# Kernel tuning notes

Measured on AMD Instinct MI355X. Metric: run time of the kernel, lower is better.

## Reference

```python
import jax, jax.numpy as jnp
import numpy as np

HEADS = 8
DIM_HEAD = 64
SCALE = DIM_HEAD ** (-0.5)


def setup_inputs() -> dict:
    key = jax.random.key(0)
    k1, k2, k3 = jax.random.split(key, 3)
    b, l, c = 8, 4096, 512
    x = jax.random.normal(k1, (b, l, c), dtype=jnp.float32)
    w_qkv = jax.random.normal(k2, (3 * c, c), dtype=jnp.float32) * (c ** -0.5)
    w_out = jax.random.normal(k3, (c, c), dtype=jnp.float32) * (c ** -0.5)
    b_out = jnp.zeros((c,), dtype=jnp.float32)
    return {"x": x, "w_qkv": w_qkv, "w_out": w_out, "b_out": b_out}


def reference(x, w_qkv, w_out, b_out):
    b, l, c = x.shape
    h = HEADS
    lh = l // h
    # to_qkv: Linear(dim, 3*dim, bias=False)
    qkv = x @ w_qkv.T                                   # (b, l, 3c)
    qkv = qkv.reshape(b, lh, h, 3, c).transpose(3, 0, 2, 1, 4)  # (3, b, h, l/h, c)
    q, k, v = qkv[0], qkv[1], qkv[2]                    # each (b, h, l/h, c)
    # transpose(-2,-1): attention is over the CHANNEL axis
    q = jnp.swapaxes(q, -2, -1)                         # (b, h, c, l/h)
    k = jnp.swapaxes(k, -2, -1)                         # (b, h, c, l/h)
    v = jnp.swapaxes(v, -2, -1)                         # (b, h, c, l/h)
    attn = jnp.einsum('bhcl,bhdl->bhcd', q, k) * SCALE  # (b, h, c, c)
    attn = jax.nn.softmax(attn, axis=-1)
    y = jnp.einsum('bhcd,bhdl->bhcl', attn, v)          # (b, h, c, l/h)
    y = y.transpose(0, 3, 1, 2).reshape(b, l, c)        # (b, l/h, h, c) -> (b, l, c)
    # to_out: Linear(dim, dim) + Dropout (identity at eval)
    out = y @ w_out.T + b_out
    return out
```

## Files before the change

kernel.cpp:

```cpp
#include <hip/hip_runtime.h>
#include <stdint.h>
#include <stddef.h>

typedef _Float16 f16;
typedef _Float16 f16x8 __attribute__((ext_vector_type(8)));
typedef _Float16 f16x4 __attribute__((ext_vector_type(4)));
typedef float f32x4 __attribute__((ext_vector_type(4)));

__device__ __forceinline__ void gload16(const void* g, void* l) {
    auto gp = (const __attribute__((address_space(1))) uint32_t*)(uintptr_t)g;
    auto lp = (__attribute__((address_space(3))) uint32_t*)(uintptr_t)l;
    __builtin_amdgcn_global_load_lds(gp, lp, 16, 0, 0);
}

__device__ __forceinline__ f16x4 cvt4(f32x4 v) {
    return f16x4{ (f16)v[0], (f16)v[1], (f16)v[2], (f16)v[3] };
}

__global__ __launch_bounds__(256) void prep_k(const float* __restrict__ x,
                                              const float* __restrict__ wqkv,
                                              const float* __restrict__ wout,
                                              f16* __restrict__ xb,
                                              f16* __restrict__ wqb,
                                              f16* __restrict__ wob) {
    int tid = blockIdx.x * blockDim.x + threadIdx.x;
    int stride = gridDim.x * blockDim.x;
    for (int i = tid; i < 4194304; i += stride) {
        float4 v = ((const float4*)x)[i];
        *(f16x4*)(xb + (size_t)i * 4) = f16x4{ (f16)v.x, (f16)v.y, (f16)v.z, (f16)v.w };
    }
    for (int i = tid; i < 196608; i += stride) {
        float4 v = ((const float4*)wqkv)[i];
        *(f16x4*)(wqb + (size_t)i * 4) = f16x4{ (f16)v.x, (f16)v.y, (f16)v.z, (f16)v.w };
    }
    for (int i = tid; i < 65536; i += stride) {
        float4 v = ((const float4*)wout)[i];
        *(f16x4*)(wob + (size_t)i * 4) = f16x4{ (f16)v.x, (f16)v.y, (f16)v.z, (f16)v.w };
    }
}


#define STAGE(NB) do {                                                          \
    gload16(Ab + kb + sE,          &ldsA[NB][( 0 + wid*8)*64]);                 \
    gload16(Ab + kb + sO + 32768,  &ldsA[NB][(32 + wid*8)*64]);                 \
    gload16(Ab + kb + sE + 65536,  &ldsA[NB][(64 + wid*8)*64]);                 \
    gload16(Ab + kb + sO + 98304,  &ldsA[NB][(96 + wid*8)*64]);                 \
    gload16(Bb + kb + sE,          &ldsB[NB][( 0 + wid*8)*64]);                 \
    gload16(Bb + kb + sO + 32768,  &ldsB[NB][(32 + wid*8)*64]);                 \
    gload16(Bb + kb + sE + 65536,  &ldsB[NB][(64 + wid*8)*64]);                 \
    gload16(Bb + kb + sO + 98304,  &ldsB[NB][(96 + wid*8)*64]);                 \
    kb += 128;                                                                  \
} while (0)

#define RD(SET, BUF) do {                                                       \
    _Pragma("unroll") for (int mi = 0; mi < 4; ++mi)                            \
    _Pragma("unroll") for (int kk = 0; kk < 2; ++kk)                            \
        aF##SET[mi][kk] = *(const f16x8*)(&ldsA[BUF][0] + aoff[mi][kk]);        \
    _Pragma("unroll") for (int ni = 0; ni < 4; ++ni)                            \
    _Pragma("unroll") for (int kk = 0; kk < 2; ++kk)                            \
        bF##SET[ni][kk] = *(const f16x8*)(&ldsB[BUF][0] + boff[ni][kk]);        \
} while (0)

#define MM(SET, KK, ML, MH_) do {                                               \
    __builtin_amdgcn_s_setprio(1);                                              \
    _Pragma("unroll") for (int mi = ML; mi < MH_; ++mi)                         \
    _Pragma("unroll") for (int ni = 0; ni < 4; ++ni) {                          \
        if constexpr (SWP)                                                      \
            acc[mi][ni] = __builtin_amdgcn_mfma_f32_16x16x32_f16(               \
                bF##SET[ni][KK], aF##SET[mi][KK], acc[mi][ni], 0, 0, 0);        \
        else                                                                    \
            acc[mi][ni] = __builtin_amdgcn_mfma_f32_16x16x32_f16(               \
                aF##SET[mi][KK], bF##SET[ni][KK], acc[mi][ni], 0, 0, 0);        \
    }                                                                           \
    __builtin_amdgcn_s_setprio(0);                                              \
} while (0)

#define MM3(SET)   do { MM(SET, 0, 0, 2); MM(SET, 0, 2, 4); MM(SET, 1, 0, 2); } while (0)
#define MMLAST(SET) MM(SET, 1, 2, 4)
#define W0  asm volatile("s_waitcnt vmcnt(0)" ::: "memory")
#define BAR __builtin_amdgcn_s_barrier()

#define TILE(CUR, NXT, NB, STG, FINAL) do {                                     \
    if (STG) STAGE(NB);                                                         \
    MM3(CUR);                                                                   \
    if (!FINAL) { W0; BAR; RD(NXT, NB); }                                       \
    MMLAST(CUR);                                                                \
} while (0)

template <int MODE, bool SWP, bool QK>
__global__ __launch_bounds__(256, 2) void g10_k(const f16* __restrict__ A0,
                                                const f16* __restrict__ B0,
                                                void* __restrict__ C0,
                                                void* __restrict__ C1,
                                                const float* __restrict__ bias) {
    __shared__ f16 ldsA[2][8192];
    __shared__ f16 ldsB[2][8192];

    const int tid = threadIdx.x;
    const int lane = tid & 63;
    const int wid = tid >> 6;
    const int wr = wid >> 1;
    const int wc = wid & 1;

    const int bid = blockIdx.x;
    int tm, tn, bh = 0;
    if constexpr (MODE == 0 && QK) {
        int swz = (bid & 7) * 256 + (bid >> 3);
        tm = (swz >> 3) * 128; tn = (swz & 7) * 128;
    } else if constexpr (MODE == 0) {
        int swz = (bid & 7) * 128 + (bid >> 3);
        tm = (swz >> 2) * 128; tn = (swz & 3) * 128;
    } else if constexpr (MODE == 1 || MODE == 2) {
        int swz = (bid & 7) * 128 + (bid >> 3);
        bh = swz >> 4; tm = ((swz >> 2) & 3) * 128; tn = (swz & 3) * 128;
    } else {
        int swz = (bid & 7) * 128 + (bid >> 3);
        tm = (swz >> 2) * 128; tn = (swz & 3) * 128;
    }

    const size_t bhoff = (MODE == 1 || MODE == 2) ? (size_t)bh * 262144 : 0;
    const char* Ab = (const char*)(A0 + bhoff + (size_t)tm * 512);
    const char* Bb = (const char*)(B0 + bhoff + (size_t)tn * 512);

    const int u = tid >> 3;
    const int colE = ((tid & 7) ^ ((u & 7) ^ (u >> 3))) * 16;
    const int sE = u * 1024 + colE;
    const int sO = sE ^ 64;
    int kb = 0;

    int aoff[4][2], boff[4][2];
#pragma unroll
    for (int mi = 0; mi < 4; ++mi) {
        int r;
        if constexpr (QK) {
            r = (lane & 15) * 8 + wr * 4 + mi;
        } else {
            r = wr * 64 + mi * 16 + (lane & 15);
        }
#pragma unroll
        for (int kk = 0; kk < 2; ++kk) {
            int c8 = (lane >> 4) + kk * 4;
            aoff[mi][kk] = r * 64 + (c8 ^ ((r & 7) ^ ((r >> 3) & 7))) * 8;
        }
    }
#pragma unroll
    for (int ni = 0; ni < 4; ++ni) {
        int r = wc * 64 + ni * 16 + (lane & 15);
#pragma unroll
        for (int kk = 0; kk < 2; ++kk) {
            int c8 = (lane >> 4) + kk * 4;
            boff[ni][kk] = r * 64 + (c8 ^ ((r & 7) ^ ((r >> 3) & 7))) * 8;
        }
    }

    f32x4 acc[4][4] = {};
    f16x8 aF0[4][2], bF0[4][2], aF1[4][2], bF1[4][2];

    STAGE(0);
    W0; BAR;
    RD(0, 0);

#pragma unroll 1
    for (int i = 0; i < 3; ++i) {
        TILE(0, 1, 1, true, false);
        TILE(1, 0, 0, true, false);
    }
    TILE(0, 1, 1, true, false);
    TILE(1, 1, 1, false, true);

    if constexpr (MODE == 0 && QK) {
        const int b = tm >> 12;
        const int lt = (tm & 4095) >> 3;
        f16* dst = (f16*)(tn < 512 ? C0 : C1);
        const int cb = (tn & 511) + wc * 64;
        const int lh0 = lt + (lane >> 4) * 4;
#pragma unroll
        for (int mi = 0; mi < 4; ++mi) {
            int h = wr * 4 + mi;
#pragma unroll
            for (int ni = 0; ni < 4; ++ni) {
                int c = cb + ni * 16 + (lane & 15);
                *(f16x4*)(dst + ((size_t)((b * 8 + h) * 512 + c)) * 512 + lh0) =
                    cvt4(acc[mi][ni]);
            }
        }
    } else if constexpr (MODE == 0) {
        f16* dst = (f16*)C0;
#pragma unroll
        for (int mi = 0; mi < 4; ++mi) {
            int t = tm + wr * 64 + mi * 16 + (lane & 15);
            int b = t >> 12, l = t & 4095;
            int h = l & 7, lh = l >> 3;
#pragma unroll
            for (int ni = 0; ni < 4; ++ni) {
                int d0 = tn + wc * 64 + ni * 16 + (lane >> 4) * 4;
                *(f16x4*)(dst + ((size_t)((b * 8 + h) * 512 + lh)) * 512 + d0) =
                    cvt4(acc[mi][ni]);
            }
        }
    } else if constexpr (MODE == 1) {
        f16* S = (f16*)C0 + (size_t)bh * 262144;
#pragma unroll
        for (int mi = 0; mi < 4; ++mi) {
            int cm = tm + wr * 64 + mi * 16 + (lane & 15);
#pragma unroll
            for (int ni = 0; ni < 4; ++ni) {
                int d0 = tn + wc * 64 + ni * 16 + (lane >> 4) * 4;
                *(f16x4*)(S + (size_t)cm * 512 + d0) = cvt4(acc[mi][ni] * 0.125f);
            }
        }
    } else if constexpr (MODE == 2) {
        f16* yb = (f16*)C0;
        const int b = bh >> 3, h = bh & 7;
#pragma unroll
        for (int mi = 0; mi < 4; ++mi) {
            int c0 = tm + wr * 64 + mi * 16 + (lane >> 4) * 4;
#pragma unroll
            for (int ni = 0; ni < 4; ++ni) {
                int l = tn + wc * 64 + ni * 16 + (lane & 15);
                size_t tok = (size_t)b * 4096 + (size_t)l * 8 + h;
                *(f16x4*)(yb + tok * 512 + c0) = cvt4(acc[mi][ni]);
            }
        }
    } else {
        float* O = (float*)C0;
#pragma unroll
        for (int mi = 0; mi < 4; ++mi) {
            int m = tm + wr * 64 + mi * 16 + (lane & 15);
#pragma unroll
            for (int ni = 0; ni < 4; ++ni) {
                int n0 = tn + wc * 64 + ni * 16 + (lane >> 4) * 4;
                float4 bv = *(const float4*)(bias + n0);
                f32x4 v = acc[mi][ni];
                v[0] += bv.x; v[1] += bv.y; v[2] += bv.z; v[3] += bv.w;
                *(f32x4*)(O + (size_t)m * 512 + n0) = v;
            }
        }
    }
}

__global__ __launch_bounds__(256) void softmax_k(const f16* __restrict__ S,
                                                 f16* __restrict__ P) {
    int row = blockIdx.x * 4 + (threadIdx.x >> 6);
    int lane = threadIdx.x & 63;
    f16x8 v = *(const f16x8*)(S + (size_t)row * 512 + lane * 8);
    float f[8];
#pragma unroll
    for (int i = 0; i < 8; ++i) f[i] = (float)v[i];
    float m = f[0];
#pragma unroll
    for (int i = 1; i < 8; ++i) m = fmaxf(m, f[i]);
#pragma unroll
    for (int off = 1; off < 64; off <<= 1) m = fmaxf(m, __shfl_xor(m, off, 64));
    float s = 0.f, e[8];
#pragma unroll
    for (int i = 0; i < 8; ++i) { e[i] = __expf(f[i] - m); s += e[i]; }
#pragma unroll
    for (int off = 1; off < 64; off <<= 1) s += __shfl_xor(s, off, 64);
    float inv = 1.0f / s;
    f16x8 pk;
#pragma unroll
    for (int i = 0; i < 8; ++i) pk[i] = (f16)(e[i] * inv);
    *(f16x8*)(P + (size_t)row * 512 + lane * 8) = pk;
}

extern "C" void kernel_launch(void* const* d_in, const int* in_sizes, int n_in,
                              void* d_out, int out_size, void* d_ws, size_t ws_size,
                              hipStream_t stream) {
    const float* x = (const float*)d_in[0];
    const float* wqkv = (const float*)d_in[1];
    const float* wout = (const float*)d_in[2];
    const float* bout = (const float*)d_in[3];
    float* out = (float*)d_out;
    char* ws = (char*)d_ws;
    const size_t MBs = 1u << 20;

    f16* xb  = (f16*)(ws + 0);
    f16* wqb = (f16*)(ws + 32 * MBs);
    f16* wob = (f16*)(ws + 34 * MBs);
    f16* Qb  = (f16*)(ws + 35 * MBs);
    f16* Kb  = (f16*)(ws + 67 * MBs);
    f16* Vb  = (f16*)(ws + 99 * MBs);
    f16* Sb  = (f16*)(ws + 131 * MBs);
    f16* Pb  = xb;
    f16* yb  = Qb;

    prep_k<<<1024, 256, 0, stream>>>(x, wqkv, wout, xb, wqb, wob);
    g10_k<0, false, true><<<2048, 256, 0, stream>>>(xb, wqb, Qb, Kb, nullptr);
    g10_k<0, true, false><<<1024, 256, 0, stream>>>(xb, wqb + (size_t)1024 * 512, Vb, nullptr, nullptr);
    g10_k<1, true, false><<<1024, 256, 0, stream>>>(Qb, Kb, Sb, nullptr, nullptr);
    softmax_k<<<8192, 256, 0, stream>>>(Sb, Pb);
    g10_k<2, false, false><<<1024, 256, 0, stream>>>(Pb, Vb, yb, nullptr, nullptr);
    g10_k<3, true, false><<<1024, 256, 0, stream>>>(yb, wob, out, nullptr, bout);
}
```

Measured before the change: 198.3 us.

## Enlarge GEMM tiles to 256x256 with 512-thread blocks and simplify pipeline

```diff
diff --git a/kernel.cpp b/kernel.cpp
--- a/kernel.cpp
+++ b/kernel.cpp
@@ -41,142 +41,131 @@
 
 
 #define STAGE(NB) do {                                                          \
-    gload16(Ab + kb + sE,          &ldsA[NB][( 0 + wid*8)*64]);                 \
-    gload16(Ab + kb + sO + 32768,  &ldsA[NB][(32 + wid*8)*64]);                 \
-    gload16(Ab + kb + sE + 65536,  &ldsA[NB][(64 + wid*8)*64]);                 \
-    gload16(Ab + kb + sO + 98304,  &ldsA[NB][(96 + wid*8)*64]);                 \
-    gload16(Bb + kb + sE,          &ldsB[NB][( 0 + wid*8)*64]);                 \
-    gload16(Bb + kb + sO + 32768,  &ldsB[NB][(32 + wid*8)*64]);                 \
-    gload16(Bb + kb + sE + 65536,  &ldsB[NB][(64 + wid*8)*64]);                 \
-    gload16(Bb + kb + sO + 98304,  &ldsB[NB][(96 + wid*8)*64]);                 \
-    kb += 128;                                                                  \
-} while (0)
-
-#define RD(SET, BUF) do {                                                       \
-    _Pragma("unroll") for (int mi = 0; mi < 4; ++mi)                            \
-    _Pragma("unroll") for (int kk = 0; kk < 2; ++kk)                            \
-        aF##SET[mi][kk] = *(const f16x8*)(&ldsA[BUF][0] + aoff[mi][kk]);        \
+    gload16(At + soff,          &ldsA[NB][(  0 + wid*8)*64]);                   \
+    gload16(At + soff + 65536,  &ldsA[NB][( 64 + wid*8)*64]);                   \
+    gload16(At + soff + 131072, &ldsA[NB][(128 + wid*8)*64]);                   \
+    gload16(At + soff + 196608, &ldsA[NB][(192 + wid*8)*64]);                   \
+    gload16(Bt + soff,          &ldsB[NB][(  0 + wid*8)*64]);                   \
+    gload16(Bt + soff + 65536,  &ldsB[NB][( 64 + wid*8)*64]);                   \
+    gload16(Bt + soff + 131072, &ldsB[NB][(128 + wid*8)*64]);                   \
+    gload16(Bt + soff + 196608, &ldsB[NB][(192 + wid*8)*64]);                   \
+    At += 128; Bt += 128;                                                       \
+} while (0)
+
+#define RD(BUF) do {                                                            \
     _Pragma("unroll") for (int ni = 0; ni < 4; ++ni)                            \
     _Pragma("unroll") for (int kk = 0; kk < 2; ++kk)                            \
-        bF##SET[ni][kk] = *(const f16x8*)(&ldsB[BUF][0] + boff[ni][kk]);        \
-} while (0)
-
-#define MM(SET, KK, ML, MH_) do {                                               \
+        bF[ni][kk] = *(const f16x8*)(&ldsB[BUF][0] + boff[ni] + kk * 32);       \
+    _Pragma("unroll") for (int mi = 0; mi < 8; ++mi)                            \
+    _Pragma("unroll") for (int kk = 0; kk < 2; ++kk)                            \
+        aF[mi][kk] = *(const f16x8*)(&ldsA[BUF][0] + aoff[mi] + kk * 32);       \
+} while (0)
+
+#define MM do {                                                                 \
     __builtin_amdgcn_s_setprio(1);                                              \
-    _Pragma("unroll") for (int mi = ML; mi < MH_; ++mi)                         \
-    _Pragma("unroll") for (int ni = 0; ni < 4; ++ni) {                          \
+    _Pragma("unroll") for (int mi = 0; mi < 8; ++mi)                            \
+    _Pragma("unroll") for (int ni = 0; ni < 4; ++ni)                            \
+    _Pragma("unroll") for (int kk = 0; kk < 2; ++kk) {                          \
         if constexpr (SWP)                                                      \
             acc[mi][ni] = __builtin_amdgcn_mfma_f32_16x16x32_f16(               \
-                bF##SET[ni][KK], aF##SET[mi][KK], acc[mi][ni], 0, 0, 0);        \
+                bF[ni][kk], aF[mi][kk], acc[mi][ni], 0, 0, 0);                  \
         else                                                                    \
             acc[mi][ni] = __builtin_amdgcn_mfma_f32_16x16x32_f16(               \
-                aF##SET[mi][KK], bF##SET[ni][KK], acc[mi][ni], 0, 0, 0);        \
+                aF[mi][kk], bF[ni][kk], acc[mi][ni], 0, 0, 0);                  \
     }                                                                           \
     __builtin_amdgcn_s_setprio(0);                                              \
 } while (0)
 
-#define MM3(SET)   do { MM(SET, 0, 0, 2); MM(SET, 0, 2, 4); MM(SET, 1, 0, 2); } while (0)
-#define MMLAST(SET) MM(SET, 1, 2, 4)
 #define W0  asm volatile("s_waitcnt vmcnt(0)" ::: "memory")
 #define BAR __builtin_amdgcn_s_barrier()
 
-#define TILE(CUR, NXT, NB, STG, FINAL) do {                                     \
+#define TILE(CB, NB, STG, FINAL) do {                                           \
     if (STG) STAGE(NB);                                                         \
-    MM3(CUR);                                                                   \
-    if (!FINAL) { W0; BAR; RD(NXT, NB); }                                       \
-    MMLAST(CUR);                                                                \
+    RD(CB);                                                                     \
+    MM;                                                                         \
+    if (!FINAL) { W0; BAR; }                                                    \
 } while (0)
 
 template <int MODE, bool SWP, bool QK>
-__global__ __launch_bounds__(256, 2) void g10_k(const f16* __restrict__ A0,
+__global__ __launch_bounds__(512, 2) void g11_k(const f16* __restrict__ A0,
                                                 const f16* __restrict__ B0,
                                                 void* __restrict__ C0,
                                                 void* __restrict__ C1,
                                                 const float* __restrict__ bias) {
-    __shared__ f16 ldsA[2][8192];
-    __shared__ f16 ldsB[2][8192];
+    __shared__ f16 ldsA[2][16384];
+    __shared__ f16 ldsB[2][16384];
 
     const int tid = threadIdx.x;
     const int lane = tid & 63;
     const int wid = tid >> 6;
-    const int wr = wid >> 1;
-    const int wc = wid & 1;
+    const int wr = wid >> 2;
+    const int wc = wid & 3;
 
     const int bid = blockIdx.x;
     int tm, tn, bh = 0;
     if constexpr (MODE == 0 && QK) {
-        int swz = (bid & 7) * 256 + (bid >> 3);
-        tm = (swz >> 3) * 128; tn = (swz & 7) * 128;
+        int swz = (bid & 7) * 64 + (bid >> 3);
+        tm = (swz >> 2) * 256; tn = (swz & 3) * 256;
     } else if constexpr (MODE == 0) {
-        int swz = (bid & 7) * 128 + (bid >> 3);
-        tm = (swz >> 2) * 128; tn = (swz & 3) * 128;
+        int swz = (bid & 7) * 32 + (bid >> 3);
+        tm = (swz >> 1) * 256; tn = (swz & 1) * 256;
     } else if constexpr (MODE == 1 || MODE == 2) {
-        int swz = (bid & 7) * 128 + (bid >> 3);
-        bh = swz >> 4; tm = ((swz >> 2) & 3) * 128; tn = (swz & 3) * 128;
+        int swz = (bid & 7) * 32 + (bid >> 3);
+        bh = swz >> 2; tm = ((swz >> 1) & 1) * 256; tn = (swz & 1) * 256;
     } else {
-        int swz = (bid & 7) * 128 + (bid >> 3);
-        tm = (swz >> 2) * 128; tn = (swz & 3) * 128;
+        int swz = (bid & 7) * 32 + (bid >> 3);
+        tm = (swz >> 1) * 256; tn = (swz & 1) * 256;
     }
 
     const size_t bhoff = (MODE == 1 || MODE == 2) ? (size_t)bh * 262144 : 0;
-    const char* Ab = (const char*)(A0 + bhoff + (size_t)tm * 512);
-    const char* Bb = (const char*)(B0 + bhoff + (size_t)tn * 512);
-
-    const int u = tid >> 3;
-    const int colE = ((tid & 7) ^ ((u & 7) ^ (u >> 3))) * 16;
-    const int sE = u * 1024 + colE;
-    const int sO = sE ^ 64;
-    int kb = 0;
-
-    int aoff[4][2], boff[4][2];
-#pragma unroll
-    for (int mi = 0; mi < 4; ++mi) {
+    const char* At = (const char*)(A0 + bhoff + (size_t)tm * 512);
+    const char* Bt = (const char*)(B0 + bhoff + (size_t)tn * 512);
+
+    const int soff = wid * 8192 + (lane >> 3) * 1024 +
+                     (((lane & 7) ^ ((lane >> 3) & 3) ^ (wid & 3)) * 16);
+
+    int aoff[8], boff[4];
+#pragma unroll
+    for (int mi = 0; mi < 8; ++mi) {
         int r;
         if constexpr (QK) {
-            r = (lane & 15) * 8 + wr * 4 + mi;
+            r = wr * 128 + (lane & 15) * 8 + mi;
         } else {
-            r = wr * 64 + mi * 16 + (lane & 15);
-        }
-#pragma unroll
-        for (int kk = 0; kk < 2; ++kk) {
-            int c8 = (lane >> 4) + kk * 4;
-            aoff[mi][kk] = r * 64 + (c8 ^ ((r & 7) ^ ((r >> 3) & 7))) * 8;
-        }
+            r = wr * 128 + mi * 16 + (lane & 15);
+        }
+        int s2 = (r & 3) ^ ((r >> 3) & 3);
+        aoff[mi] = r * 64 + (((lane >> 4) ^ s2)) * 8;
     }
 #pragma unroll
     for (int ni = 0; ni < 4; ++ni) {
         int r = wc * 64 + ni * 16 + (lane & 15);
-#pragma unroll
-        for (int kk = 0; kk < 2; ++kk) {
-            int c8 = (lane >> 4) + kk * 4;
-            boff[ni][kk] = r * 64 + (c8 ^ ((r & 7) ^ ((r >> 3) & 7))) * 8;
-        }
-    }
-
-    f32x4 acc[4][4] = {};
-    f16x8 aF0[4][2], bF0[4][2], aF1[4][2], bF1[4][2];
+        int s2 = (r & 3) ^ ((r >> 3) & 3);
+        boff[ni] = r * 64 + (((lane >> 4) ^ s2)) * 8;
+    }
+
+    f32x4 acc[8][4] = {};
+    f16x8 aF[8][2], bF[4][2];
 
     STAGE(0);
     W0; BAR;
-    RD(0, 0);
 
 #pragma unroll 1
     for (int i = 0; i < 3; ++i) {
-        TILE(0, 1, 1, true, false);
-        TILE(1, 0, 0, true, false);
-    }
-    TILE(0, 1, 1, true, false);
-    TILE(1, 1, 1, false, true);
+        TILE(0, 1, true, false);
+        TILE(1, 0, true, false);
+    }
+    TILE(0, 1, true, false);
+    TILE(1, 1, false, true);
 
     if constexpr (MODE == 0 && QK) {
         const int b = tm >> 12;
         const int lt = (tm & 4095) >> 3;
         f16* dst = (f16*)(tn < 512 ? C0 : C1);
         const int cb = (tn & 511) + wc * 64;
-        const int lh0 = lt + (lane >> 4) * 4;
-#pragma unroll
-        for (int mi = 0; mi < 4; ++mi) {
-            int h = wr * 4 + mi;
+        const int lh0 = lt + wr * 16 + (lane >> 4) * 4;
+#pragma unroll
+        for (int mi = 0; mi < 8; ++mi) {
+            int h = mi;
 #pragma unroll
             for (int ni = 0; ni < 4; ++ni) {
                 int c = cb + ni * 16 + (lane & 15);
@@ -187,8 +176,8 @@
     } else if constexpr (MODE == 0) {
         f16* dst = (f16*)C0;
 #pragma unroll
-        for (int mi = 0; mi < 4; ++mi) {
-            int t = tm + wr * 64 + mi * 16 + (lane & 15);
+        for (int mi = 0; mi < 8; ++mi) {
+            int t = tm + wr * 128 + mi * 16 + (lane & 15);
             int b = t >> 12, l = t & 4095;
             int h = l & 7, lh = l >> 3;
 #pragma unroll
@@ -201,8 +190,8 @@
     } else if constexpr (MODE == 1) {
         f16* S = (f16*)C0 + (size_t)bh * 262144;
 #pragma unroll
-        for (int mi = 0; mi < 4; ++mi) {
-            int cm = tm + wr * 64 + mi * 16 + (lane & 15);
+        for (int mi = 0; mi < 8; ++mi) {
+            int cm = tm + wr * 128 + mi * 16 + (lane & 15);
 #pragma unroll
             for (int ni = 0; ni < 4; ++ni) {
                 int d0 = tn + wc * 64 + ni * 16 + (lane >> 4) * 4;
@@ -213,8 +202,8 @@
         f16* yb = (f16*)C0;
         const int b = bh >> 3, h = bh & 7;
 #pragma unroll
-        for (int mi = 0; mi < 4; ++mi) {
-            int c0 = tm + wr * 64 + mi * 16 + (lane >> 4) * 4;
+        for (int mi = 0; mi < 8; ++mi) {
+            int c0 = tm + wr * 128 + mi * 16 + (lane >> 4) * 4;
 #pragma unroll
             for (int ni = 0; ni < 4; ++ni) {
                 int l = tn + wc * 64 + ni * 16 + (lane & 15);
@@ -225,8 +214,8 @@
     } else {
         float* O = (float*)C0;
 #pragma unroll
-        for (int mi = 0; mi < 4; ++mi) {
-            int m = tm + wr * 64 + mi * 16 + (lane & 15);
+        for (int mi = 0; mi < 8; ++mi) {
+            int m = tm + wr * 128 + mi * 16 + (lane & 15);
 #pragma unroll
             for (int ni = 0; ni < 4; ++ni) {
                 int n0 = tn + wc * 64 + ni * 16 + (lane >> 4) * 4;
@@ -286,10 +275,10 @@
     f16* yb  = Qb;
 
     prep_k<<<1024, 256, 0, stream>>>(x, wqkv, wout, xb, wqb, wob);
-    g10_k<0, false, true><<<2048, 256, 0, stream>>>(xb, wqb, Qb, Kb, nullptr);
-    g10_k<0, true, false><<<1024, 256, 0, stream>>>(xb, wqb + (size_t)1024 * 512, Vb, nullptr, nullptr);
-    g10_k<1, true, false><<<1024, 256, 0, stream>>>(Qb, Kb, Sb, nullptr, nullptr);
+    g11_k<0, false, true><<<512, 512, 0, stream>>>(xb, wqb, Qb, Kb, nullptr);
+    g11_k<0, true, false><<<256, 512, 0, stream>>>(xb, wqb + (size_t)1024 * 512, Vb, nullptr, nullptr);
+    g11_k<1, true, false><<<256, 512, 0, stream>>>(Qb, Kb, Sb, nullptr, nullptr);
     softmax_k<<<8192, 256, 0, stream>>>(Sb, Pb);
-    g10_k<2, false, false><<<1024, 256, 0, stream>>>(Pb, Vb, yb, nullptr, nullptr);
-    g10_k<3, true, false><<<1024, 256, 0, stream>>>(yb, wob, out, nullptr, bout);
-}
+    g11_k<2, false, false><<<256, 512, 0, stream>>>(Pb, Vb, yb, nullptr, nullptr);
+    g11_k<3, true, false><<<256, 512, 0, stream>>>(yb, wob, out, nullptr, bout);
+}
```

Result: no change. 201.6 us (+1.7%).

## Use 256x256 tile, 512-thread GEMM kernel for QK, PV and output projection

Applied to the files above, without the earlier changes.

```diff
diff --git a/kernel.cpp b/kernel.cpp
--- a/kernel.cpp
+++ b/kernel.cpp
@@ -40,7 +40,7 @@
 }
 
 
-#define STAGE(NB) do {                                                          \
+#define A_STAGE(NB) do {                                                        \
     gload16(Ab + kb + sE,          &ldsA[NB][( 0 + wid*8)*64]);                 \
     gload16(Ab + kb + sO + 32768,  &ldsA[NB][(32 + wid*8)*64]);                 \
     gload16(Ab + kb + sE + 65536,  &ldsA[NB][(64 + wid*8)*64]);                 \
@@ -52,7 +52,7 @@
     kb += 128;                                                                  \
 } while (0)
 
-#define RD(SET, BUF) do {                                                       \
+#define A_RD(SET, BUF) do {                                                     \
     _Pragma("unroll") for (int mi = 0; mi < 4; ++mi)                            \
     _Pragma("unroll") for (int kk = 0; kk < 2; ++kk)                            \
         aF##SET[mi][kk] = *(const f16x8*)(&ldsA[BUF][0] + aoff[mi][kk]);        \
@@ -61,7 +61,7 @@
         bF##SET[ni][kk] = *(const f16x8*)(&ldsB[BUF][0] + boff[ni][kk]);        \
 } while (0)
 
-#define MM(SET, KK, ML, MH_) do {                                               \
+#define A_MM(SET, KK, ML, MH_) do {                                             \
     __builtin_amdgcn_s_setprio(1);                                              \
     _Pragma("unroll") for (int mi = ML; mi < MH_; ++mi)                         \
     _Pragma("unroll") for (int ni = 0; ni < 4; ++ni) {                          \
@@ -75,16 +75,16 @@
     __builtin_amdgcn_s_setprio(0);                                              \
 } while (0)
 
-#define MM3(SET)   do { MM(SET, 0, 0, 2); MM(SET, 0, 2, 4); MM(SET, 1, 0, 2); } while (0)
-#define MMLAST(SET) MM(SET, 1, 2, 4)
+#define A_MM3(SET)   do { A_MM(SET, 0, 0, 2); A_MM(SET, 0, 2, 4); A_MM(SET, 1, 0, 2); } while (0)
+#define A_MMLAST(SET) A_MM(SET, 1, 2, 4)
 #define W0  asm volatile("s_waitcnt vmcnt(0)" ::: "memory")
 #define BAR __builtin_amdgcn_s_barrier()
 
-#define TILE(CUR, NXT, NB, STG, FINAL) do {                                     \
-    if (STG) STAGE(NB);                                                         \
-    MM3(CUR);                                                                   \
-    if (!FINAL) { W0; BAR; RD(NXT, NB); }                                       \
-    MMLAST(CUR);                                                                \
+#define A_TILE(CUR, NXT, NB, STG, FINAL) do {                                   \
+    if (STG) A_STAGE(NB);                                                       \
+    A_MM3(CUR);                                                                 \
+    if (!FINAL) { W0; BAR; A_RD(NXT, NB); }                                     \
+    A_MMLAST(CUR);                                                              \
 } while (0)
 
 template <int MODE, bool SWP, bool QK>
@@ -103,24 +103,17 @@
     const int wc = wid & 1;
 
     const int bid = blockIdx.x;
-    int tm, tn, bh = 0;
+    int tm, tn;
     if constexpr (MODE == 0 && QK) {
         int swz = (bid & 7) * 256 + (bid >> 3);
         tm = (swz >> 3) * 128; tn = (swz & 7) * 128;
-    } else if constexpr (MODE == 0) {
-        int swz = (bid & 7) * 128 + (bid >> 3);
-        tm = (swz >> 2) * 128; tn = (swz & 3) * 128;
-    } else if constexpr (MODE == 1 || MODE == 2) {
-        int swz = (bid & 7) * 128 + (bid >> 3);
-        bh = swz >> 4; tm = ((swz >> 2) & 3) * 128; tn = (swz & 3) * 128;
     } else {
         int swz = (bid & 7) * 128 + (bid >> 3);
         tm = (swz >> 2) * 128; tn = (swz & 3) * 128;
     }
 
-    const size_t bhoff = (MODE == 1 || MODE == 2) ? (size_t)bh * 262144 : 0;
-    const char* Ab = (const char*)(A0 + bhoff + (size_t)tm * 512);
-    const char* Bb = (const char*)(B0 + bhoff + (size_t)tn * 512);
+    const char* Ab = (const char*)(A0 + (size_t)tm * 512);
+    const char* Bb = (const char*)(B0 + (size_t)tn * 512);
 
     const int u = tid >> 3;
     const int colE = ((tid & 7) ^ ((u & 7) ^ (u >> 3))) * 16;
@@ -156,17 +149,17 @@
     f32x4 acc[4][4] = {};
     f16x8 aF0[4][2], bF0[4][2], aF1[4][2], bF1[4][2];
 
-    STAGE(0);
+    A_STAGE(0);
     W0; BAR;
-    RD(0, 0);
+    A_RD(0, 0);
 
 #pragma unroll 1
     for (int i = 0; i < 3; ++i) {
-        TILE(0, 1, 1, true, false);
-        TILE(1, 0, 0, true, false);
-    }
-    TILE(0, 1, 1, true, false);
-    TILE(1, 1, 1, false, true);
+        A_TILE(0, 1, 1, true, false);
+        A_TILE(1, 0, 0, true, false);
+    }
+    A_TILE(0, 1, 1, true, false);
+    A_TILE(1, 1, 1, false, true);
 
     if constexpr (MODE == 0 && QK) {
         const int b = tm >> 12;
@@ -184,7 +177,7 @@
                     cvt4(acc[mi][ni]);
             }
         }
-    } else if constexpr (MODE == 0) {
+    } else {
         f16* dst = (f16*)C0;
 #pragma unroll
         for (int mi = 0; mi < 4; ++mi) {
@@ -198,11 +191,120 @@
                     cvt4(acc[mi][ni]);
             }
         }
-    } else if constexpr (MODE == 1) {
+    }
+}
+
+
+#define B_STAGE(NB) do {                                                        \
+    gload16(At + soff,          &ldsA[NB][(  0 + wid*8)*64]);                   \
+    gload16(At + soff + 65536,  &ldsA[NB][( 64 + wid*8)*64]);                   \
+    gload16(At + soff + 131072, &ldsA[NB][(128 + wid*8)*64]);                   \
+    gload16(At + soff + 196608, &ldsA[NB][(192 + wid*8)*64]);                   \
+    gload16(Bt + soff,          &ldsB[NB][(  0 + wid*8)*64]);                   \
+    gload16(Bt + soff + 65536,  &ldsB[NB][( 64 + wid*8)*64]);                   \
+    gload16(Bt + soff + 131072, &ldsB[NB][(128 + wid*8)*64]);                   \
+    gload16(Bt + soff + 196608, &ldsB[NB][(192 + wid*8)*64]);                   \
+    At += 128; Bt += 128;                                                       \
+} while (0)
+
+#define B_RD12(KK, BUF) do {                                                    \
+    _Pragma("unroll") for (int ni = 0; ni < 4; ++ni)                            \
+        bF[ni] = *(const f16x8*)(&ldsB[BUF][0] + boff[ni][KK]);                 \
+    _Pragma("unroll") for (int mi = 0; mi < 8; ++mi)                            \
+        aF[mi] = *(const f16x8*)(&ldsA[BUF][0] + aoff[mi][KK]);                 \
+} while (0)
+
+#define B_MM32 do {                                                             \
+    __builtin_amdgcn_s_setprio(1);                                              \
+    _Pragma("unroll") for (int mi = 0; mi < 8; ++mi)                            \
+    _Pragma("unroll") for (int ni = 0; ni < 4; ++ni) {                          \
+        if constexpr (SWP)                                                      \
+            acc[mi][ni] = __builtin_amdgcn_mfma_f32_16x16x32_f16(               \
+                bF[ni], aF[mi], acc[mi][ni], 0, 0, 0);                          \
+        else                                                                    \
+            acc[mi][ni] = __builtin_amdgcn_mfma_f32_16x16x32_f16(               \
+                aF[mi], bF[ni], acc[mi][ni], 0, 0, 0);                          \
+    }                                                                           \
+    __builtin_amdgcn_s_setprio(0);                                              \
+} while (0)
+
+#define B_TILE(CB, NB, STG, FINAL) do {                                         \
+    B_RD12(0, CB);                                                              \
+    if (STG) B_STAGE(NB);                                                       \
+    B_MM32;                                                                     \
+    B_RD12(1, CB);                                                              \
+    B_MM32;                                                                     \
+    if (!FINAL) { W0; BAR; }                                                    \
+} while (0)
+
+template <int MODE, bool SWP>
+__global__ __launch_bounds__(512) void g12_k(const f16* __restrict__ A0,
+                                             const f16* __restrict__ B0,
+                                             void* __restrict__ C0,
+                                             const float* __restrict__ bias) {
+    __shared__ f16 ldsA[2][16384];
+    __shared__ f16 ldsB[2][16384];
+
+    const int tid = threadIdx.x;
+    const int lane = tid & 63;
+    const int wid = tid >> 6;
+    const int wr = wid >> 2;
+    const int wc = wid & 3;
+
+    const int bid = blockIdx.x;
+    int tm, tn, bh = 0;
+    if constexpr (MODE == 1 || MODE == 2) {
+        int swz = (bid & 7) * 32 + (bid >> 3);
+        bh = swz >> 2; tm = ((swz >> 1) & 1) * 256; tn = (swz & 1) * 256;
+    } else {
+        int swz = (bid & 7) * 32 + (bid >> 3);
+        tm = (swz >> 1) * 256; tn = (swz & 1) * 256;
+    }
+
+    const size_t bhoff = (MODE == 1 || MODE == 2) ? (size_t)bh * 262144 : 0;
+    const char* At = (const char*)(A0 + bhoff + (size_t)tm * 512);
+    const char* Bt = (const char*)(B0 + bhoff + (size_t)tn * 512);
+
+    const int soff = wid * 8192 + (lane >> 3) * 1024 +
+                     ((((lane & 7) ^ (lane >> 3) ^ wid) & 7) * 16);
+
+    int aoff[8][2], boff[4][2];
+#pragma unroll
+    for (int mi = 0; mi < 8; ++mi) {
+        int r = wr * 128 + mi * 16 + (lane & 15);
+        int s3 = (r & 7) ^ ((r >> 3) & 7);
+#pragma unroll
+        for (int kk = 0; kk < 2; ++kk)
+            aoff[mi][kk] = r * 64 + ((((lane >> 4) + kk * 4) ^ s3)) * 8;
+    }
+#pragma unroll
+    for (int ni = 0; ni < 4; ++ni) {
+        int r = wc * 64 + ni * 16 + (lane & 15);
+        int s3 = (r & 7) ^ ((r >> 3) & 7);
+#pragma unroll
+        for (int kk = 0; kk < 2; ++kk)
+            boff[ni][kk] = r * 64 + ((((lane >> 4) + kk * 4) ^ s3)) * 8;
+    }
+
+    f32x4 acc[8][4] = {};
+    f16x8 aF[8], bF[4];
+
+    B_STAGE(0);
+    W0; BAR;
+
+#pragma unroll 1
+    for (int i = 0; i < 3; ++i) {
+        B_TILE(0, 1, true, false);
+        B_TILE(1, 0, true, false);
+    }
+    B_TILE(0, 1, true, false);
+    B_TILE(1, 1, false, true);
+
+    if constexpr (MODE == 1) {
         f16* S = (f16*)C0 + (size_t)bh * 262144;
 #pragma unroll
-        for (int mi = 0; mi < 4; ++mi) {
-            int cm = tm + wr * 64 + mi * 16 + (lane & 15);
+        for (int mi = 0; mi < 8; ++mi) {
+            int cm = tm + wr * 128 + mi * 16 + (lane & 15);
 #pragma unroll
             for (int ni = 0; ni < 4; ++ni) {
                 int d0 = tn + wc * 64 + ni * 16 + (lane >> 4) * 4;
@@ -213,8 +315,8 @@
         f16* yb = (f16*)C0;
         const int b = bh >> 3, h = bh & 7;
 #pragma unroll
-        for (int mi = 0; mi < 4; ++mi) {
-            int c0 = tm + wr * 64 + mi * 16 + (lane >> 4) * 4;
+        for (int mi = 0; mi < 8; ++mi) {
+            int c0 = tm + wr * 128 + mi * 16 + (lane >> 4) * 4;
 #pragma unroll
             for (int ni = 0; ni < 4; ++ni) {
                 int l = tn + wc * 64 + ni * 16 + (lane & 15);
@@ -225,8 +327,8 @@
     } else {
         float* O = (float*)C0;
 #pragma unroll
-        for (int mi = 0; mi < 4; ++mi) {
-            int m = tm + wr * 64 + mi * 16 + (lane & 15);
+        for (int mi = 0; mi < 8; ++mi) {
+            int m = tm + wr * 128 + mi * 16 + (lane & 15);
 #pragma unroll
             for (int ni = 0; ni < 4; ++ni) {
                 int n0 = tn + wc * 64 + ni * 16 + (lane >> 4) * 4;
@@ -288,8 +390,8 @@
     prep_k<<<1024, 256, 0, stream>>>(x, wqkv, wout, xb, wqb, wob);
     g10_k<0, false, true><<<2048, 256, 0, stream>>>(xb, wqb, Qb, Kb, nullptr);
     g10_k<0, true, false><<<1024, 256, 0, stream>>>(xb, wqb + (size_t)1024 * 512, Vb, nullptr, nullptr);
-    g10_k<1, true, false><<<1024, 256, 0, stream>>>(Qb, Kb, Sb, nullptr, nullptr);
+    g12_k<1, true><<<256, 512, 0, stream>>>(Qb, Kb, Sb, nullptr);
     softmax_k<<<8192, 256, 0, stream>>>(Sb, Pb);
-    g10_k<2, false, false><<<1024, 256, 0, stream>>>(Pb, Vb, yb, nullptr, nullptr);
-    g10_k<3, true, false><<<1024, 256, 0, stream>>>(yb, wob, out, nullptr, bout);
-}
+    g12_k<2, false><<<256, 512, 0, stream>>>(Pb, Vb, yb, nullptr);
+    g12_k<3, true><<<256, 512, 0, stream>>>(yb, wob, out, bout);
+}
```

Result: faster. 191.8 us (-3.2%).
